# Optimization experiments

Measured on AMD Instinct MI355X. Metric: run time of the kernel, lower is better.

The kernel has to match this reference:

```python
import jax, jax.numpy as jnp
import numpy as np

N = 100000
E = 3200000
NFEAT, NHID, NCLASS = 512, 256, 64


def spmm(rows, cols, vals, dense):
    # sparse [N,N] @ dense [N,D] via gather + segment-sum scatter
    gathered = dense[cols] * vals[:, None]          # [E, D]
    return jax.ops.segment_sum(gathered, rows, num_segments=N)


def setup_inputs() -> dict:
    key = jax.random.key(0)
    ks = jax.random.split(key, 12)
    x = jax.random.normal(ks[0], (N, NFEAT), dtype=jnp.float32)
    adj1_rows = jax.random.randint(ks[1], (E,), 0, N)
    adj1_cols = jax.random.randint(ks[2], (E,), 0, N)
    adj1_vals = jax.random.uniform(ks[3], (E,), dtype=jnp.float32)
    adj2_rows = jax.random.randint(ks[4], (E,), 0, N)
    adj2_cols = jax.random.randint(ks[5], (E,), 0, N)
    adj2_vals = jax.random.uniform(ks[6], (E,), dtype=jnp.float32)
    # Kipf-style uniform init for GraphConvolution weights
    std1 = 1.0 / np.sqrt(NHID)
    std2 = 1.0 / np.sqrt(NCLASS)
    W1 = jax.random.uniform(ks[7], (NFEAT, NHID), minval=-std1, maxval=std1, dtype=jnp.float32)
    b1 = jax.random.uniform(ks[8], (NHID,), minval=-std1, maxval=std1, dtype=jnp.float32)
    W2 = jax.random.uniform(ks[9], (NHID, NCLASS), minval=-std2, maxval=std2, dtype=jnp.float32)
    b2 = jax.random.uniform(ks[10], (NCLASS,), minval=-std2, maxval=std2, dtype=jnp.float32)
    return {
        "x": x,
        "adj1_rows": adj1_rows, "adj1_cols": adj1_cols, "adj1_vals": adj1_vals,
        "adj2_rows": adj2_rows, "adj2_cols": adj2_cols, "adj2_vals": adj2_vals,
        "W1": W1, "b1": b1, "W2": W2, "b2": b2,
    }


def reference(x, adj1_rows, adj1_cols, adj1_vals, adj2_rows, adj2_cols, adj2_vals, W1, b1, W2, b2):
    # layer 1: support = x @ W1 ; h = adj1 @ support + b1
    h = spmm(adj1_rows, adj1_cols, adj1_vals, x @ W1) + b1
    h = jax.nn.relu(h)
    # dropout is identity in eval mode
    # layer 2
    out = spmm(adj2_rows, adj2_cols, adj2_vals, h @ W2) + b2
    return jax.nn.log_softmax(out, axis=1)
```

## Files before the change

### kernel.cpp

```cpp
#include <hip/hip_runtime.h>
#include <hip/hip_fp8.h>
#include <cstdint>

#define NFEAT 512
#define NHID 256
#define NCLASS 64
#define RPB 256
#define MAXBUK 512
#define TEDG 2048
#define CAP 9216
#define PAD 16

typedef __attribute__((ext_vector_type(8))) short bf16x8;
typedef __attribute__((ext_vector_type(4))) float f32x4;
typedef unsigned long long ull;

__device__ __forceinline__ unsigned short f2bf(float f) {
  unsigned u = __builtin_bit_cast(unsigned, f);
  u = (u + 0x7FFF + ((u >> 16) & 1)) >> 16;
  return (unsigned short)u;
}
__device__ __forceinline__ float bfu(unsigned short u) {
  return __builtin_bit_cast(float, (unsigned)u << 16);
}
__device__ __forceinline__ unsigned char f2fp8(float f) {
  __hip_fp8_e4m3 t(f);
  return (unsigned char)t.__x;
}
__device__ __forceinline__ float fp82f(unsigned char u) {
  __hip_fp8_e4m3 t; t.__x = u;
  return (float)t;
}

__global__ __launch_bounds__(256)
void init_k(const float* __restrict__ W1, short* __restrict__ W1T,
            const float* __restrict__ W2, short* __restrict__ W2T,
            int* __restrict__ tailp, int nbuk) {
  const int idx = blockIdx.x * 256 + threadIdx.x;
  if (idx < 512 * 256) {
    const int k = idx >> 8, n = idx & 255;
    W1T[n * 512 + k] = (short)f2bf(W1[idx]);
  } else if (idx < 512 * 256 + 256 * 64) {
    const int j = idx - 512 * 256;
    const int k = j >> 6, n = j & 63;
    W2T[n * 256 + k] = (short)f2bf(W2[j]);
  } else {
    const int j = idx - 512 * 256 - 256 * 64;
    if (j < 2 * nbuk) tailp[j * PAD] = (j % nbuk) * CAP;
  }
}

#define ASTR 40
__global__ __launch_bounds__(256)
void gemm1_mfma(const float* __restrict__ A, const short* __restrict__ BT,
                unsigned char* __restrict__ C, int M) {
  __shared__ short As[128 * ASTR];
  const int t    = threadIdx.x;
  const int w    = t >> 6;
  const int lane = t & 63;
  const int lr   = lane & 15;
  const int g    = lane >> 4;
  const int bm   = blockIdx.x * 128;

  f32x4 acc[8][4] = {};
  float4 f0[2], f1[2];

#pragma unroll
  for (int p = 0; p < 2; ++p) {
    const int gran = p * 256 + t;
    const int row  = gran >> 2;
    const int kc   = (gran & 3) << 3;
    const int grow = bm + row;
    f0[p] = make_float4(0.f, 0.f, 0.f, 0.f); f1[p] = f0[p];
    if (grow < M) {
      const float* src = A + (size_t)grow * NFEAT + kc;
      f0[p] = *(const float4*)(src);
      f1[p] = *(const float4*)(src + 4);
    }
  }

  for (int k0 = 0; k0 < NFEAT; k0 += 32) {
#pragma unroll
    for (int p = 0; p < 2; ++p) {
      const int gran = p * 256 + t;
      const int row  = gran >> 2;
      const int kc   = (gran & 3) << 3;
      union { bf16x8 v; unsigned short u[8]; } pk;
      pk.u[0] = f2bf(f0[p].x); pk.u[1] = f2bf(f0[p].y); pk.u[2] = f2bf(f0[p].z); pk.u[3] = f2bf(f0[p].w);
      pk.u[4] = f2bf(f1[p].x); pk.u[5] = f2bf(f1[p].y); pk.u[6] = f2bf(f1[p].z); pk.u[7] = f2bf(f1[p].w);
      *(bf16x8*)(&As[row * ASTR + kc]) = pk.v;
    }
    __syncthreads();

    if (k0 + 32 < NFEAT) {
#pragma unroll
      for (int p = 0; p < 2; ++p) {
        const int gran = p * 256 + t;
        const int row  = gran >> 2;
        const int kc   = (gran & 3) << 3;
        const int grow = bm + row;
        f0[p] = make_float4(0.f, 0.f, 0.f, 0.f); f1[p] = f0[p];
        if (grow < M) {
          const float* src = A + (size_t)grow * NFEAT + (k0 + 32) + kc;
          f0[p] = *(const float4*)(src);
          f1[p] = *(const float4*)(src + 4);
        }
      }
    }

    bf16x8 bfr[4];
#pragma unroll
    for (int n = 0; n < 4; ++n) {
      const int col = w * 64 + n * 16 + lr;
      bfr[n] = *(const bf16x8*)(BT + (size_t)col * NFEAT + k0 + g * 8);
    }
#pragma unroll
    for (int m = 0; m < 8; ++m) {
      const bf16x8 af = *(const bf16x8*)(&As[(m * 16 + lr) * ASTR + g * 8]);
#pragma unroll
      for (int n = 0; n < 4; ++n)
        acc[m][n] = __builtin_amdgcn_mfma_f32_16x16x32_bf16(af, bfr[n], acc[m][n], 0, 0, 0);
    }
    __syncthreads();
  }

#pragma unroll
  for (int m = 0; m < 8; ++m) {
#pragma unroll
    for (int r = 0; r < 4; ++r) {
      const int row = bm + m * 16 + g * 4 + r;
      if (row < M) {
#pragma unroll
        for (int n = 0; n < 4; ++n) {
          const int col = w * 64 + n * 16 + lr;
          C[(size_t)row * NHID + col] = f2fp8(acc[m][n][r]);
        }
      }
    }
  }
}

__global__ __launch_bounds__(256)
void gemm2_mfma(const unsigned short* __restrict__ A, const short* __restrict__ BT,
                unsigned short* __restrict__ C, int M) {
  __shared__ short As[128 * 32];
  const int t    = threadIdx.x;
  const int w    = t >> 6;
  const int lane = t & 63;
  const int lr   = lane & 15;
  const int g    = lane >> 4;
  const int bm   = blockIdx.x * 128;

  f32x4 acc[2][4] = {};

  for (int k0 = 0; k0 < NHID; k0 += 32) {
#pragma unroll
    for (int p = 0; p < 2; ++p) {
      const int gran = p * 256 + t;
      const int row  = gran >> 2;
      const int kc   = (gran & 3) << 3;
      const int grow = bm + row;
      bf16x8 av = {};
      if (grow < M) av = *(const bf16x8*)(A + (size_t)grow * NHID + k0 + kc);
      *(bf16x8*)(&As[gran * 8]) = av;
    }
    __syncthreads();

    bf16x8 bfr[4];
#pragma unroll
    for (int n = 0; n < 4; ++n) {
      const int col = n * 16 + lr;
      bfr[n] = *(const bf16x8*)(BT + (size_t)col * NHID + k0 + g * 8);
    }
#pragma unroll
    for (int m = 0; m < 2; ++m) {
      const bf16x8 af = *(const bf16x8*)(&As[(w * 32 + m * 16 + lr) * 32 + g * 8]);
#pragma unroll
      for (int n = 0; n < 4; ++n)
        acc[m][n] = __builtin_amdgcn_mfma_f32_16x16x32_bf16(af, bfr[n], acc[m][n], 0, 0, 0);
    }
    __syncthreads();
  }

#pragma unroll
  for (int m = 0; m < 2; ++m) {
#pragma unroll
    for (int r = 0; r < 4; ++r) {
      const int row = bm + w * 32 + m * 16 + g * 4 + r;
      if (row < M) {
#pragma unroll
        for (int n = 0; n < 4; ++n) {
          const int col = n * 16 + lr;
          C[(size_t)row * NCLASS + col] = f2bf(acc[m][n][r]);
        }
      }
    }
  }
}


__global__ __launch_bounds__(256)
void bucket_append_k(const int* __restrict__ r1, const int* __restrict__ c1, const float* __restrict__ v1,
                     const int* __restrict__ r2, const int* __restrict__ c2, const float* __restrict__ v2,
                     int* __restrict__ tailp,
                     ull* __restrict__ ecvP1, ull* __restrict__ ecvP2,
                     int nbuk, int E1, int E2) {
  __shared__ ull stage[TEDG];
  __shared__ unsigned short sbk[TEDG];
  __shared__ int cnt[MAXBUK], rsv[MAXBUK], cur[MAXBUK], off2[MAXBUK];
  __shared__ int wsum[4];
  const int a = blockIdx.y;
  const int* rows = a ? r2 : r1;
  const int* cols = a ? c2 : c1;
  const float* vals = a ? v2 : v1;
  ull* ecvP = a ? ecvP2 : ecvP1;
  const int E = a ? E2 : E1;
  const int e0 = blockIdx.x * TEDG;
  if (e0 >= E) return;
  const int e1 = min(E, e0 + TEDG);
  const int n = e1 - e0;
  const int t = threadIdx.x;
  const int lane = t & 63;

  for (int b = t; b < MAXBUK; b += 256) cnt[b] = 0;
  __syncthreads();
  for (int i = e0 + t; i < e1; i += 256)
    atomicAdd(&cnt[rows[i] >> 8], 1);
  __syncthreads();

  const int c0 = cnt[2 * t], c1b = cnt[2 * t + 1];
  int s = c0 + c1b;
#pragma unroll
  for (int o = 1; o < 64; o <<= 1) {
    const int x = __shfl_up(s, o);
    if (lane >= o) s += x;
  }
  const int wv = t >> 6;
  if (lane == 63) wsum[wv] = s;
  __syncthreads();
  int wo = 0;
#pragma unroll
  for (int k = 0; k < 4; ++k) if (k < wv) wo += wsum[k];
  const int ex = wo + s - (c0 + c1b);
  off2[2 * t] = ex;
  off2[2 * t + 1] = ex + c0;
  cur[2 * t] = ex;
  cur[2 * t + 1] = ex + c0;
  for (int b = t; b < nbuk; b += 256) {
    const int c = cnt[b];
    if (c) rsv[b] = atomicAdd(&tailp[(a * nbuk + b) * PAD], c);
  }
  __syncthreads();

  for (int i = e0 + t; i < e1; i += 256) {
    const int r = rows[i];
    const int b = r >> 8;
    const int pos = atomicAdd(&cur[b], 1);
    stage[pos] = ((ull)__builtin_bit_cast(unsigned, vals[i]) << 32)
               | ((unsigned)(r & 255) << 17) | (unsigned)cols[i];
    sbk[pos] = (unsigned short)b;
  }
  __syncthreads();

  for (int j = t; j < n; j += 256) {
    const int b = sbk[j];
    ecvP[(size_t)rsv[b] + (j - off2[b])] = stage[j];
  }
}

__global__ __launch_bounds__(256)
void bucket_scan_k(const int* __restrict__ tailp, int* __restrict__ base,
                   int* __restrict__ row_ptr, int nbuk, int M, int E1, int E2) {
  __shared__ int pair[256];
  const int a = blockIdx.x;
  const int E = a ? E2 : E1;
  const int t = threadIdx.x;
  const int b0 = t * 2, b1 = t * 2 + 1;
  const int v0 = (b0 < nbuk) ? (tailp[(a * nbuk + b0) * PAD] - b0 * CAP) : 0;
  const int v1 = (b1 < nbuk) ? (tailp[(a * nbuk + b1) * PAD] - b1 * CAP) : 0;
  pair[t] = v0 + v1;
  __syncthreads();
  for (int off = 1; off < 256; off <<= 1) {
    const int x = (t >= off) ? pair[t - off] : 0;
    __syncthreads();
    pair[t] += x;
    __syncthreads();
  }
  const int excl = pair[t] - (v0 + v1);
  if (b0 < nbuk) base[a * (nbuk + 1) + b0] = excl;
  if (b1 < nbuk) base[a * (nbuk + 1) + b1] = excl + v0;
  if (t == 0) { base[a * (nbuk + 1) + nbuk] = E; row_ptr[(size_t)a * (M + 1) + M] = E; }
}

__global__ __launch_bounds__(256)
void bucket_csr_k(const ull* __restrict__ ecvP1, const ull* __restrict__ ecvP2,
                  const int* __restrict__ base, int* __restrict__ row_ptr,
                  ull* __restrict__ ecv1, ull* __restrict__ ecv2,
                  int nbuk, int M) {
  __shared__ int hist[RPB], excl[RPB], cur[RPB];
  const int b = blockIdx.x, a = blockIdx.y;
  const ull* src = (a ? ecvP2 : ecvP1) + (size_t)b * CAP;
  ull* dst = a ? ecv2 : ecv1;
  const int s = base[a * (nbuk + 1) + b];
  const int e = base[a * (nbuk + 1) + b + 1];
  const int n = e - s;
  const int t = threadIdx.x;
  hist[t] = 0;
  __syncthreads();
  for (int i = t; i < n; i += 256) {
    const unsigned lo = (unsigned)src[i];
    atomicAdd(&hist[(lo >> 17) & 255], 1);
  }
  __syncthreads();
  const int v = hist[t];
  excl[t] = v;
  __syncthreads();
  for (int off = 1; off < 256; off <<= 1) {
    const int x = (t >= off) ? excl[t - off] : 0;
    __syncthreads();
    excl[t] += x;
    __syncthreads();
  }
  const int ex = excl[t] - v;
  const int r = b * RPB + t;
  if (r < M) row_ptr[(size_t)a * (M + 1) + r] = s + ex;
  cur[t] = s + ex;
  __syncthreads();
  for (int i = t; i < n; i += 256) {
    const ull pk = src[i];
    const unsigned lo = (unsigned)pk;
    const int rl = (lo >> 17) & 255;
    const int pos = atomicAdd(&cur[rl], 1);
    dst[pos] = (pk & 0xFFFFFFFF00000000ULL) | (lo & 0x1FFFFu);
  }
}

__global__ __launch_bounds__(256)
void spmm1_fp8_k(const int* __restrict__ rp, const ull* __restrict__ ecv,
                 const unsigned char* __restrict__ dense, const float* __restrict__ bias,
                 unsigned short* __restrict__ out, int M) {
  const int wid = (blockIdx.x * 256 + threadIdx.x) >> 6;
  if (wid >= M) return;
  const int lane = threadIdx.x & 63;
  const int d4 = lane << 2;
  const int start = rp[wid], end = rp[wid + 1];
  float4 acc  = *(const float4*)(bias + d4);
  float4 acc2 = make_float4(0.f, 0.f, 0.f, 0.f);
  for (int j0 = start; j0 < end; j0 += 64) {
    const int jm = min(64, end - j0);
    const int jr = (jm + 7) & ~7;
    const ull pk = (lane < jm) ? __builtin_nontemporal_load(ecv + j0 + lane) : 0ULL;
    for (int kk = 0; kk < jr; kk += 8) {
#pragma unroll
      for (int u = 0; u < 8; ++u) {
        const ull pp = __shfl(pk, kk + u);
        const int   cc = (int)(unsigned)pp & 0x1FFFF;
        const float vv = __builtin_bit_cast(float, (unsigned)(pp >> 32));
        const uchar4 g8 = *(const uchar4*)(dense + ((size_t)cc << 8) + d4);
        const float gx = fp82f(g8.x), gy = fp82f(g8.y), gz = fp82f(g8.z), gw = fp82f(g8.w);
        if (u & 1) {
          acc2.x += vv * gx; acc2.y += vv * gy; acc2.z += vv * gz; acc2.w += vv * gw;
        } else {
          acc.x += vv * gx; acc.y += vv * gy; acc.z += vv * gz; acc.w += vv * gw;
        }
      }
    }
  }
  acc.x += acc2.x; acc.y += acc2.y; acc.z += acc2.z; acc.w += acc2.w;
  union { ushort4 o4; ull u64; } o;
  o.o4.x = f2bf(fmaxf(acc.x, 0.f));
  o.o4.y = f2bf(fmaxf(acc.y, 0.f));
  o.o4.z = f2bf(fmaxf(acc.z, 0.f));
  o.o4.w = f2bf(fmaxf(acc.w, 0.f));
  __builtin_nontemporal_store(o.u64, (ull*)(out + (size_t)wid * NHID + d4));
}

__global__ __launch_bounds__(256)
void spmm_csr_d64_lsm_bf(const int* __restrict__ rp, const ull* __restrict__ ecv,
                         const unsigned short* __restrict__ dense,
                         const float* __restrict__ bias, float* __restrict__ out, int M) {
  const int wid = (blockIdx.x * 256 + threadIdx.x) >> 6;
  if (wid >= M) return;
  const int lane = threadIdx.x & 63;
  const int start = rp[wid], end = rp[wid + 1];
  float acc0 = bias[lane], acc1 = 0.f;
  for (int j0 = start; j0 < end; j0 += 64) {
    const int jm = min(64, end - j0);
    const int jr = (jm + 7) & ~7;
    const ull pk = (lane < jm) ? __builtin_nontemporal_load(ecv + j0 + lane) : 0ULL;
    for (int kk = 0; kk < jr; kk += 8) {
#pragma unroll
      for (int u = 0; u < 8; ++u) {
        const ull pp = __shfl(pk, kk + u);
        const int   cc = (int)(unsigned)pp & 0x1FFFF;
        const float vv = __builtin_bit_cast(float, (unsigned)(pp >> 32));
        const float gv = bfu(dense[(size_t)cc * NCLASS + lane]);
        if (u & 1) acc1 += vv * gv; else acc0 += vv * gv;
      }
    }
  }
  const float acc = acc0 + acc1;
  float m = acc;
#pragma unroll
  for (int off = 32; off; off >>= 1) m = fmaxf(m, __shfl_xor(m, off));
  const float e = __expf(acc - m);
  float s = e;
#pragma unroll
  for (int off = 32; off; off >>= 1) s += __shfl_xor(s, off);
  out[(size_t)wid * NCLASS + lane] = acc - m - __logf(s);
}

static inline size_t align256(size_t x) { return (x + 255) & ~(size_t)255; }

extern "C" void kernel_launch(void* const* d_in, const int* in_sizes, int n_in,
                              void* d_out, int out_size, void* d_ws, size_t ws_size,
                              hipStream_t stream) {
  const float* x   = (const float*)d_in[0];
  const int*   a1r = (const int*)d_in[1];
  const int*   a1c = (const int*)d_in[2];
  const float* a1v = (const float*)d_in[3];
  const int*   a2r = (const int*)d_in[4];
  const int*   a2c = (const int*)d_in[5];
  const float* a2v = (const float*)d_in[6];
  const float* W1  = (const float*)d_in[7];
  const float* b1  = (const float*)d_in[8];
  const float* W2  = (const float*)d_in[9];
  const float* b2  = (const float*)d_in[10];
  float* out = (float*)d_out;

  const int M  = in_sizes[0] / NFEAT;
  const int E1 = in_sizes[1];
  const int E2 = in_sizes[4];
  const int Emax = (E1 > E2) ? E1 : E2;
  const int nbuk = (M + RPB - 1) / RPB;
  const int ntiles = (Emax + TEDG - 1) / TEDG;
  const int nbG = (M + 127) / 128;

  char* p = (char*)d_ws;
  unsigned char* s1   = (unsigned char*)p;          p += align256((size_t)M * NHID);
  unsigned short* h   = (unsigned short*)p;         p += align256((size_t)M * NHID * sizeof(short));
  unsigned short* s2  = (unsigned short*)p;         p += align256((size_t)M * NCLASS * sizeof(short));
  short* W1T          = (short*)p;                  p += align256((size_t)NFEAT * NHID * sizeof(short));
  short* W2T          = (short*)p;                  p += align256((size_t)NHID * NCLASS * sizeof(short));
  ull* ecvP1          = (ull*)p;                    p += align256((size_t)nbuk * CAP * 8);
  ull* ecvP2          = (ull*)p;                    p += align256((size_t)nbuk * CAP * 8);
  ull* ecv1           = (ull*)p;                    p += align256((size_t)E1 * 8);
  ull* ecv2           = (ull*)p;                    p += align256((size_t)E2 * 8);
  int*   row_ptr      = (int*)p;                    p += align256((size_t)2 * (M + 1) * sizeof(int));
  int*   bkt_base     = (int*)p;                    p += align256((size_t)2 * (nbuk + 1) * sizeof(int));
  int*   tailp        = (int*)p;                    p += align256((size_t)2 * nbuk * PAD * sizeof(int));

  const int blkRow = (M * 64 + 255) / 256;

  {
    const int total = 512 * 256 + 256 * 64 + 2 * nbuk;
    init_k<<<(total + 255) / 256, 256, 0, stream>>>(W1, W1T, W2, W2T, tailp, nbuk);
  }
  {
    dim3 gA(ntiles, 2);
    bucket_append_k<<<gA, 256, 0, stream>>>(a1r, a1c, a1v, a2r, a2c, a2v,
                                            tailp, ecvP1, ecvP2, nbuk, E1, E2);
    bucket_scan_k<<<2, 256, 0, stream>>>(tailp, bkt_base, row_ptr, nbuk, M, E1, E2);
    dim3 gC(nbuk, 2);
    bucket_csr_k<<<gC, 256, 0, stream>>>(ecvP1, ecvP2, bkt_base, row_ptr, ecv1, ecv2, nbuk, M);
  }
  gemm1_mfma<<<nbG, 256, 0, stream>>>(x, W1T, s1, M);
  spmm1_fp8_k<<<blkRow, 256, 0, stream>>>(row_ptr, ecv1, s1, b1, h, M);
  gemm2_mfma<<<nbG, 256, 0, stream>>>(h, W2T, s2, M);
  spmm_csr_d64_lsm_bf<<<blkRow, 256, 0, stream>>>(row_ptr + (M + 1), ecv2, s2, b2, out, M);
}
```

Baseline: 559.7 us.

## Preload edge tiles into registers and double bucketing tile size

The bucketing kernel now loads each thread's rows, cols and vals into registers once, up front, with all loads issued together. Before, rows were read twice and cols/vals were read inside the atomic scatter loop. The edge tile per block doubles, which halves the number of blocks and the per-bucket global tail atomics, and doubles the shared staging buffer. Costs are higher register pressure (48 values per thread) and shared memory use, which may lower occupancy.

```diff
diff --git a/kernel.cpp b/kernel.cpp
--- a/kernel.cpp
+++ b/kernel.cpp
@@ -7,7 +7,8 @@
 #define NCLASS 64
 #define RPB 256
 #define MAXBUK 512
-#define TEDG 2048
+#define TEDG 4096
+#define EPT 16
 #define CAP 9216
 #define PAD 16
 
@@ -222,10 +223,26 @@
   const int t = threadIdx.x;
   const int lane = t & 63;
 
+  int   rreg[EPT];
+  int   creg[EPT];
+  float vreg[EPT];
+#pragma unroll
+  for (int j = 0; j < EPT; ++j) {
+    const int i = e0 + j * 256 + t;
+    rreg[j] = (i < e1) ? rows[i] : -1;
+  }
+#pragma unroll
+  for (int j = 0; j < EPT; ++j) {
+    const int i = e0 + j * 256 + t;
+    if (i < e1) { creg[j] = cols[i]; vreg[j] = vals[i]; }
+    else        { creg[j] = 0;       vreg[j] = 0.f; }
+  }
+
   for (int b = t; b < MAXBUK; b += 256) cnt[b] = 0;
   __syncthreads();
-  for (int i = e0 + t; i < e1; i += 256)
-    atomicAdd(&cnt[rows[i] >> 8], 1);
+#pragma unroll
+  for (int j = 0; j < EPT; ++j)
+    if (rreg[j] >= 0) atomicAdd(&cnt[rreg[j] >> 8], 1);
   __syncthreads();
 
   const int c0 = cnt[2 * t], c1b = cnt[2 * t + 1];
@@ -252,13 +269,16 @@
   }
   __syncthreads();
 
-  for (int i = e0 + t; i < e1; i += 256) {
-    const int r = rows[i];
-    const int b = r >> 8;
-    const int pos = atomicAdd(&cur[b], 1);
-    stage[pos] = ((ull)__builtin_bit_cast(unsigned, vals[i]) << 32)
-               | ((unsigned)(r & 255) << 17) | (unsigned)cols[i];
-    sbk[pos] = (unsigned short)b;
+#pragma unroll
+  for (int j = 0; j < EPT; ++j) {
+    const int r = rreg[j];
+    if (r >= 0) {
+      const int b = r >> 8;
+      const int pos = atomicAdd(&cur[b], 1);
+      stage[pos] = ((ull)__builtin_bit_cast(unsigned, vreg[j]) << 32)
+                 | ((unsigned)(r & 255) << 17) | (unsigned)creg[j];
+      sbk[pos] = (unsigned short)b;
+    }
   }
   __syncthreads();
 
```

New measurement: 503.2 us. 1.11x faster.
